# Kernel tuning notes

Measured on AMD Instinct MI355X. Metric: run time of the kernel, lower is better.

The kernel has to match this reference:

```python
import jax, jax.numpy as jnp
import numpy as np

N = 4096  # size of every layer (I, H1, H2, O)
EPS = 1e-5  # torch LayerNorm default


def _ln(x, g, b):
    # torch.nn.LayerNorm: biased variance, affine
    mu = jnp.mean(x)
    xc = x - mu
    v = jnp.mean(xc * xc)
    return xc * jax.lax.rsqrt(v + EPS) * g + b


def setup_inputs() -> dict:
    key = jax.random.key(0)
    ks = jax.random.split(key, 24)
    W = 0.02  # weight scale ~ uniform-init magnitude of nn.Linear at fan_in=4096
    inp = {
        "input_raw": jax.random.normal(ks[0], (N,), jnp.float32),
        "h1_prev": jax.random.normal(ks[1], (N,), jnp.float32),
        "h2_prev": jax.random.normal(ks[2], (N,), jnp.float32),
        "W_I_H1": jax.random.normal(ks[3], (N, N), jnp.float32) * W,
        "W_H1_H1": jax.random.normal(ks[4], (N, N), jnp.float32) * W,
        "W_H1_H2": jax.random.normal(ks[5], (N, N), jnp.float32) * W,
        "W_H2_H1": jax.random.normal(ks[6], (N, N), jnp.float32) * W,
        "W_H2_H2": jax.random.normal(ks[7], (N, N), jnp.float32) * W,
        "W_H1_O": jax.random.normal(ks[8], (N, N), jnp.float32) * W,
        "W_H2_O": jax.random.normal(ks[9], (N, N), jnp.float32) * W,
        "bias_h1": jax.random.normal(ks[10], (N,), jnp.float32) * 0.1,
        "bias_h2": jax.random.normal(ks[11], (N,), jnp.float32) * 0.1,
        "bias_o": jax.random.normal(ks[12], (N,), jnp.float32) * 0.1,
        "g_i": jax.random.uniform(ks[13], (N,), jnp.float32, 0.5, 1.5),
        "b_i": jax.random.normal(ks[14], (N,), jnp.float32) * 0.1,
        "g_h1": jax.random.uniform(ks[15], (N,), jnp.float32, 0.5, 1.5),
        "bln_h1": jax.random.normal(ks[16], (N,), jnp.float32) * 0.1,
        "g_h2": jax.random.uniform(ks[17], (N,), jnp.float32, 0.5, 1.5),
        "bln_h2": jax.random.normal(ks[18], (N,), jnp.float32) * 0.1,
        "g_o": jax.random.uniform(ks[19], (N,), jnp.float32, 0.5, 1.5),
        "bln_o": jax.random.normal(ks[20], (N,), jnp.float32) * 0.1,
    }
    return inp


def reference(input_raw, h1_prev, h2_prev,
              W_I_H1, W_H1_H1, W_H1_H2, W_H2_H1, W_H2_H2, W_H1_O, W_H2_O,
              bias_h1, bias_h2, bias_o,
              g_i, b_i, g_h1, bln_h1, g_h2, bln_h2, g_o, bln_o):
    # --- Phase 1: feedback accumulation + per-layer LayerNorm ---
    # I and O have no feedback -> LN(zeros) = LN bias (beta)
    i_out = b_i + input_raw                       # layers['I']: LN(0) then += input_raw
    h1_fb = _ln(W_H1_H1 @ h1_prev, g_h1, bln_h1)  # self-recurrent feedback H1->H1
    h2_fb = _ln(W_H2_H2 @ h2_prev, g_h2, bln_h2)  # self-recurrent feedback H2->H2
    o_init = bln_o                                # layers['O']: LN(zeros)

    # --- Phase 2: input-driven / feedback-only hidden activations ---
    h1_p2 = jax.nn.relu(_ln(W_I_H1 @ i_out + h1_fb + bias_h1, g_h1, bln_h1))  # 'I' in forward
    h2_p2 = jax.nn.relu(_ln(h2_fb + bias_h2, g_h2, bln_h2))                    # feedback-only

    # --- Phase 3: inter-hidden forward pass (intermediate_output OVERWRITES) ---
    h1_f = jax.nn.relu(_ln(W_H2_H1 @ h2_p2 + bias_h1, g_h1, bln_h1))
    h2_f = jax.nn.relu(_ln(W_H1_H2 @ h1_p2 + bias_h2, g_h2, bln_h2))

    # --- Output layer: sum forwards, tanh(LN(.)) ---
    o = jnp.tanh(_ln(o_init + W_H1_O @ h1_f + W_H2_O @ h2_f + bias_o, g_o, bln_o))
    return o
```

## Files before the change

### kernel.cpp

```cpp
#include <hip/hip_runtime.h>
#include <math.h>

#define NN 4096
#define NV4 1024
#define ROWS_PER_BLOCK 8
#define BLK 256


__device__ __forceinline__ float4 ld4(const float* __restrict__ p, int t) {
    return reinterpret_cast<const float4*>(p)[t];
}
__device__ __forceinline__ void st4(float* __restrict__ p, int t, float4 v) {
    reinterpret_cast<float4*>(p)[t] = v;
}
__device__ __forceinline__ float4 add4(float4 a, float4 b) {
    return make_float4(a.x + b.x, a.y + b.y, a.z + b.z, a.w + b.w);
}

__device__ __forceinline__ float2 block_reduce2(float s, float ss, float* sbuf) {
    #pragma unroll
    for (int off = 32; off > 0; off >>= 1) {
        s  += __shfl_down(s,  off, 64);
        ss += __shfl_down(ss, off, 64);
    }
    const int wave = threadIdx.x >> 6;
    const int lane = threadIdx.x & 63;
    if (lane == 0) { sbuf[wave] = s; sbuf[16 + wave] = ss; }
    __syncthreads();
    float rs = 0.f, rss = 0.f;
    if (threadIdx.x < 16) { rs = sbuf[threadIdx.x]; rss = sbuf[16 + threadIdx.x]; }
    if (wave == 0) {
        #pragma unroll
        for (int off = 8; off > 0; off >>= 1) {
            rs  += __shfl_down(rs,  off, 64);
            rss += __shfl_down(rss, off, 64);
        }
        if (lane == 0) { sbuf[0] = rs; sbuf[1] = rss; }
    }
    __syncthreads();
    float2 r = make_float2(sbuf[0], sbuf[1]);
    __syncthreads();
    return r;
}

struct LNStat { float mu, rstd; };

__device__ __forceinline__ LNStat ln_stats(float4 v, float* sbuf) {
    float s  = v.x + v.y + v.z + v.w;
    float ss = v.x * v.x + v.y * v.y + v.z * v.z + v.w * v.w;
    float2 r = block_reduce2(s, ss, sbuf);
    LNStat o;
    o.mu = r.x * (1.0f / NN);
    float var = r.y * (1.0f / NN) - o.mu * o.mu;
    o.rstd = rsqrtf(var + 1e-5f);
    return o;
}

__device__ __forceinline__ float4 ln_apply(float4 v, LNStat st, float4 g, float4 b) {
    return make_float4((v.x - st.mu) * st.rstd * g.x + b.x,
                       (v.y - st.mu) * st.rstd * g.y + b.y,
                       (v.z - st.mu) * st.rstd * g.z + b.z,
                       (v.w - st.mu) * st.rstd * g.w + b.w);
}

__device__ __forceinline__ float4 relu4(float4 v) {
    return make_float4(fmaxf(v.x, 0.f), fmaxf(v.y, 0.f), fmaxf(v.z, 0.f), fmaxf(v.w, 0.f));
}


__device__ __forceinline__ void gemv8(const float* __restrict__ W,
                                      const float4* __restrict__ xs,
                                      float* __restrict__ y) {
    const int wave = threadIdx.x >> 6;
    const int lane = threadIdx.x & 63;
    const int r0 = blockIdx.x * ROWS_PER_BLOCK + wave * 2;
    const float4* __restrict__ W0 = reinterpret_cast<const float4*>(W + (size_t)r0 * NN);
    const float4* __restrict__ W1 = W0 + NV4;
    float acc0 = 0.f, acc1 = 0.f;
    #pragma unroll
    for (int it = 0; it < 16; ++it) {
        const int j = (it << 6) + lane;
        float4 xv = xs[j];
        float4 a  = W0[j];
        float4 b  = W1[j];
        acc0 = fmaf(a.x, xv.x, acc0);
        acc0 = fmaf(a.y, xv.y, acc0);
        acc0 = fmaf(a.z, xv.z, acc0);
        acc0 = fmaf(a.w, xv.w, acc0);
        acc1 = fmaf(b.x, xv.x, acc1);
        acc1 = fmaf(b.y, xv.y, acc1);
        acc1 = fmaf(b.z, xv.z, acc1);
        acc1 = fmaf(b.w, xv.w, acc1);
    }
    #pragma unroll
    for (int off = 32; off > 0; off >>= 1) {
        acc0 += __shfl_down(acc0, off, 64);
        acc1 += __shfl_down(acc1, off, 64);
    }
    if (lane == 0) { y[r0] = acc0; y[r0 + 1] = acc1; }
}

__global__ __launch_bounds__(BLK) void gemv_stageA(
    const float* __restrict__ W_H1_H1, const float* __restrict__ h1_prev,
    const float* __restrict__ W_H2_H2, const float* __restrict__ h2_prev,
    const float* __restrict__ W_I_H1,  const float* __restrict__ input_raw,
    const float* __restrict__ b_i,
    float* __restrict__ mv1, float* __restrict__ mv2, float* __restrict__ mv3)
{
    __shared__ float4 xs[NV4];
    const float* W; const float* x; const float* xadd; float* y;
    if (blockIdx.y == 0)      { W = W_H1_H1; x = h1_prev;   xadd = nullptr; y = mv1; }
    else if (blockIdx.y == 1) { W = W_H2_H2; x = h2_prev;   xadd = nullptr; y = mv2; }
    else                      { W = W_I_H1;  x = input_raw; xadd = b_i;     y = mv3; }

    const float4* x4 = reinterpret_cast<const float4*>(x);
    if (xadd) {
        const float4* a4 = reinterpret_cast<const float4*>(xadd);
        #pragma unroll
        for (int k = 0; k < 4; ++k) {
            const int j = (k << 8) + threadIdx.x;
            xs[j] = add4(x4[j], a4[j]);
        }
    } else {
        #pragma unroll
        for (int k = 0; k < 4; ++k) {
            const int j = (k << 8) + threadIdx.x;
            xs[j] = x4[j];
        }
    }
    __syncthreads();
    gemv8(W, xs, y);
}

__global__ __launch_bounds__(BLK) void gemv_pair(
    const float* __restrict__ Wa, const float* __restrict__ xa, float* __restrict__ ya,
    const float* __restrict__ Wb, const float* __restrict__ xb, float* __restrict__ yb)
{
    __shared__ float4 xs[NV4];
    const float* W; const float* x; float* y;
    if (blockIdx.y == 0) { W = Wa; x = xa; y = ya; }
    else                 { W = Wb; x = xb; y = yb; }
    const float4* x4 = reinterpret_cast<const float4*>(x);
    #pragma unroll
    for (int k = 0; k < 4; ++k) {
        const int j = (k << 8) + threadIdx.x;
        xs[j] = x4[j];
    }
    __syncthreads();
    gemv8(W, xs, y);
}

__global__ __launch_bounds__(1024) void phase2_kernel(
    const float* __restrict__ mv1, const float* __restrict__ mv2, const float* __restrict__ mv3,
    const float* __restrict__ bias_h1, const float* __restrict__ bias_h2,
    const float* __restrict__ g_h1, const float* __restrict__ bln_h1,
    const float* __restrict__ g_h2, const float* __restrict__ bln_h2,
    float* __restrict__ h1_p2, float* __restrict__ h2_p2)
{
    __shared__ float sbuf[32];
    const int t = threadIdx.x;
    if (blockIdx.x == 0) {
        float4 g = ld4(g_h1, t), b = ld4(bln_h1, t);
        float4 v = ld4(mv1, t);
        LNStat s1 = ln_stats(v, sbuf);
        float4 fb = ln_apply(v, s1, g, b);
        float4 tt = add4(add4(ld4(mv3, t), fb), ld4(bias_h1, t));
        LNStat s2 = ln_stats(tt, sbuf);
        st4(h1_p2, t, relu4(ln_apply(tt, s2, g, b)));
    } else {
        float4 g = ld4(g_h2, t), b = ld4(bln_h2, t);
        float4 v = ld4(mv2, t);
        LNStat s1 = ln_stats(v, sbuf);
        float4 fb = ln_apply(v, s1, g, b);
        float4 tt = add4(fb, ld4(bias_h2, t));
        LNStat s2 = ln_stats(tt, sbuf);
        st4(h2_p2, t, relu4(ln_apply(tt, s2, g, b)));
    }
}

__global__ __launch_bounds__(1024) void phase3_kernel(
    const float* __restrict__ mv4, const float* __restrict__ mv5,
    const float* __restrict__ bias_h1, const float* __restrict__ bias_h2,
    const float* __restrict__ g_h1, const float* __restrict__ bln_h1,
    const float* __restrict__ g_h2, const float* __restrict__ bln_h2,
    float* __restrict__ h1_f, float* __restrict__ h2_f)
{
    __shared__ float sbuf[32];
    const int t = threadIdx.x;
    const float* mv;  const float* bias; const float* g; const float* b; float* out;
    if (blockIdx.x == 0) { mv = mv4; bias = bias_h1; g = g_h1; b = bln_h1; out = h1_f; }
    else                 { mv = mv5; bias = bias_h2; g = g_h2; b = bln_h2; out = h2_f; }
    float4 v = add4(ld4(mv, t), ld4(bias, t));
    LNStat s = ln_stats(v, sbuf);
    st4(out, t, relu4(ln_apply(v, s, ld4(g, t), ld4(b, t))));
}

__global__ __launch_bounds__(1024) void final_kernel(
    const float* __restrict__ mv6, const float* __restrict__ mv7,
    const float* __restrict__ bias_o, const float* __restrict__ bln_o,
    const float* __restrict__ g_o,
    float* __restrict__ out)
{
    __shared__ float sbuf[32];
    const int t = threadIdx.x;
    float4 v = add4(add4(ld4(bln_o, t), ld4(mv6, t)), add4(ld4(mv7, t), ld4(bias_o, t)));
    LNStat s = ln_stats(v, sbuf);
    float4 r = ln_apply(v, s, ld4(g_o, t), ld4(bln_o, t));
    st4(out, t, make_float4(tanhf(r.x), tanhf(r.y), tanhf(r.z), tanhf(r.w)));
}


extern "C" void kernel_launch(void* const* d_in, const int* in_sizes, int n_in,
                              void* d_out, int out_size, void* d_ws, size_t ws_size,
                              hipStream_t stream) {
    const float* input_raw = (const float*)d_in[0];
    const float* h1_prev   = (const float*)d_in[1];
    const float* h2_prev   = (const float*)d_in[2];
    const float* W_I_H1    = (const float*)d_in[3];
    const float* W_H1_H1   = (const float*)d_in[4];
    const float* W_H1_H2   = (const float*)d_in[5];
    const float* W_H2_H1   = (const float*)d_in[6];
    const float* W_H2_H2   = (const float*)d_in[7];
    const float* W_H1_O    = (const float*)d_in[8];
    const float* W_H2_O    = (const float*)d_in[9];
    const float* bias_h1   = (const float*)d_in[10];
    const float* bias_h2   = (const float*)d_in[11];
    const float* bias_o    = (const float*)d_in[12];
    const float* b_i       = (const float*)d_in[14];
    const float* g_h1      = (const float*)d_in[15];
    const float* bln_h1    = (const float*)d_in[16];
    const float* g_h2      = (const float*)d_in[17];
    const float* bln_h2    = (const float*)d_in[18];
    const float* g_o       = (const float*)d_in[19];
    const float* bln_o     = (const float*)d_in[20];

    float* ws    = (float*)d_ws;
    float* mv1   = ws;
    float* mv2   = ws + 1 * NN;
    float* mv3   = ws + 2 * NN;
    float* h1_p2 = ws + 3 * NN;
    float* h2_p2 = ws + 4 * NN;
    float* mv4   = ws + 5 * NN;
    float* mv5   = ws + 6 * NN;
    float* h1_f  = ws + 7 * NN;
    float* h2_f  = ws + 8 * NN;
    float* mv6   = ws + 9 * NN;
    float* mv7   = ws + 10 * NN;

    const int gx = NN / ROWS_PER_BLOCK;

    gemv_stageA<<<dim3(gx, 3), BLK, 0, stream>>>(
        W_H1_H1, h1_prev, W_H2_H2, h2_prev, W_I_H1, input_raw, b_i, mv1, mv2, mv3);

    phase2_kernel<<<2, 1024, 0, stream>>>(
        mv1, mv2, mv3, bias_h1, bias_h2, g_h1, bln_h1, g_h2, bln_h2, h1_p2, h2_p2);

    gemv_pair<<<dim3(gx, 2), BLK, 0, stream>>>(
        W_H2_H1, h2_p2, mv4, W_H1_H2, h1_p2, mv5);

    phase3_kernel<<<2, 1024, 0, stream>>>(
        mv4, mv5, bias_h1, bias_h2, g_h1, bln_h1, g_h2, bln_h2, h1_f, h2_f);

    gemv_pair<<<dim3(gx, 2), BLK, 0, stream>>>(
        W_H1_O, h1_f, mv6, W_H2_O, h2_f, mv7);

    final_kernel<<<1, 1024, 0, stream>>>(
        mv6, mv7, bias_o, bln_o, g_o, (float*)d_out);
}
```

Measured before the change: 104.2 us.

## Compute four rows per wave with batched float4 weight loads in GEMV

Restructures the GEMV inner loop so each wave handles four rows and each thread issues sixteen independent float4 weight loads per iteration before the FMAs. Each block now covers sixteen rows, halving the number of blocks and the redundant staging of the input vector into shared memory. The aim is more memory-level parallelism on the bandwidth-bound weight stream. The trade-off is higher register pressure and fewer blocks to fill the GPU.

New measurement: 114.6 us. 10.0% more time.

```diff
diff --git a/kernel.cpp b/kernel.cpp
--- a/kernel.cpp
+++ b/kernel.cpp
@@ -3,7 +3,8 @@
 
 #define NN 4096
 #define NV4 1024
-#define ROWS_PER_BLOCK 8
+#define RPW 4
+#define ROWS_PER_BLOCK 16
 #define BLK 256
 
 
@@ -68,36 +69,47 @@
 }
 
 
-__device__ __forceinline__ void gemv8(const float* __restrict__ W,
-                                      const float4* __restrict__ xs,
-                                      float* __restrict__ y) {
+__device__ __forceinline__ void gemv16(const float* __restrict__ W,
+                                       const float4* __restrict__ xs,
+                                       float* __restrict__ y) {
     const int wave = threadIdx.x >> 6;
     const int lane = threadIdx.x & 63;
-    const int r0 = blockIdx.x * ROWS_PER_BLOCK + wave * 2;
-    const float4* __restrict__ W0 = reinterpret_cast<const float4*>(W + (size_t)r0 * NN);
-    const float4* __restrict__ W1 = W0 + NV4;
-    float acc0 = 0.f, acc1 = 0.f;
-    #pragma unroll
-    for (int it = 0; it < 16; ++it) {
-        const int j = (it << 6) + lane;
-        float4 xv = xs[j];
-        float4 a  = W0[j];
-        float4 b  = W1[j];
-        acc0 = fmaf(a.x, xv.x, acc0);
-        acc0 = fmaf(a.y, xv.y, acc0);
-        acc0 = fmaf(a.z, xv.z, acc0);
-        acc0 = fmaf(a.w, xv.w, acc0);
-        acc1 = fmaf(b.x, xv.x, acc1);
-        acc1 = fmaf(b.y, xv.y, acc1);
-        acc1 = fmaf(b.z, xv.z, acc1);
-        acc1 = fmaf(b.w, xv.w, acc1);
+    const int r0 = blockIdx.x * ROWS_PER_BLOCK + wave * RPW;
+    const float4* __restrict__ Wr = reinterpret_cast<const float4*>(W) + (size_t)r0 * NV4;
+    float acc[RPW] = {0.f, 0.f, 0.f, 0.f};
+    #pragma unroll
+    for (int it = 0; it < 4; ++it) {
+        const int jb = (it << 8) + lane;
+        float4 w[RPW][4];
+        #pragma unroll
+        for (int r = 0; r < RPW; ++r) {
+            #pragma unroll
+            for (int k = 0; k < 4; ++k)
+                w[r][k] = Wr[(size_t)r * NV4 + jb + (k << 6)];
+        }
+        float4 xv[4];
+        #pragma unroll
+        for (int k = 0; k < 4; ++k) xv[k] = xs[jb + (k << 6)];
+        #pragma unroll
+        for (int r = 0; r < RPW; ++r) {
+            #pragma unroll
+            for (int k = 0; k < 4; ++k) {
+                acc[r] = fmaf(w[r][k].x, xv[k].x, acc[r]);
+                acc[r] = fmaf(w[r][k].y, xv[k].y, acc[r]);
+                acc[r] = fmaf(w[r][k].z, xv[k].z, acc[r]);
+                acc[r] = fmaf(w[r][k].w, xv[k].w, acc[r]);
+            }
+        }
     }
     #pragma unroll
     for (int off = 32; off > 0; off >>= 1) {
-        acc0 += __shfl_down(acc0, off, 64);
-        acc1 += __shfl_down(acc1, off, 64);
-    }
-    if (lane == 0) { y[r0] = acc0; y[r0 + 1] = acc1; }
+        #pragma unroll
+        for (int r = 0; r < RPW; ++r) acc[r] += __shfl_down(acc[r], off, 64);
+    }
+    if (lane == 0) {
+        #pragma unroll
+        for (int r = 0; r < RPW; ++r) y[r0 + r] = acc[r];
+    }
 }
 
 __global__ __launch_bounds__(BLK) void gemv_stageA(
@@ -129,7 +141,7 @@
         }
     }
     __syncthreads();
-    gemv8(W, xs, y);
+    gemv16(W, xs, y);
 }
 
 __global__ __launch_bounds__(BLK) void gemv_pair(
@@ -147,7 +159,7 @@
         xs[j] = x4[j];
     }
     __syncthreads();
-    gemv8(W, xs, y);
+    gemv16(W, xs, y);
 }
 
 __global__ __launch_bounds__(1024) void phase2_kernel(
```

## Double-buffer GEMV weight rows into LDS via async global-to-LDS loads

Applied to the files above, without the earlier changes.

Replaces the register-streaming GEMV with a block-wide loop that stages one weight row at a time into LDS using the global_load_lds builtin. The two LDS buffers are ping-ponged so the next row loads while the current row is dotted against x, which is held in registers. Rows per block double to 16. The aim is to overlap HBM fetches with compute and cut register-held loads. In exchange the loop needs a block barrier per row and 32KB of LDS per block, which may lower occupancy and the number of bytes in flight.

New measurement: 102.4 us. About the same (-1.7%).

```diff
diff --git a/kernel.cpp b/kernel.cpp
--- a/kernel.cpp
+++ b/kernel.cpp
@@ -2,8 +2,7 @@
 #include <math.h>
 
 #define NN 4096
-#define NV4 1024
-#define ROWS_PER_BLOCK 8
+#define ROWS_PER_BLOCK 16
 #define BLK 256
 
 
@@ -15,6 +14,39 @@
 }
 __device__ __forceinline__ float4 add4(float4 a, float4 b) {
     return make_float4(a.x + b.x, a.y + b.y, a.z + b.z, a.w + b.w);
+}
+
+typedef const __attribute__((address_space(1))) unsigned int* gas1_u32;
+typedef __attribute__((address_space(3))) unsigned int* las3_u32;
+__device__ __forceinline__ void async16(const float* g, float* l) {
+    __builtin_amdgcn_global_load_lds((gas1_u32)(const void*)g, (las3_u32)(void*)l, 16, 0, 0);
+}
+
+__device__ __forceinline__ void stage_row(const float* __restrict__ W, int row,
+                                          float* __restrict__ buf, int wave, int lane) {
+    const float* g = W + (size_t)row * NN + wave * 1024 + lane * 4;
+    float* l = buf + wave * 1024;
+    async16(g,       l);
+    async16(g + 256, l + 256);
+    async16(g + 512, l + 512);
+    async16(g + 768, l + 768);
+}
+
+__device__ __forceinline__ float dot_row(const float* __restrict__ buf,
+                                         const float4 xr[4], int tid) {
+    const float4* b4 = reinterpret_cast<const float4*>(buf);
+    float p = 0.f;
+    #pragma unroll
+    for (int i = 0; i < 4; ++i) {
+        float4 w = b4[i * 256 + tid];
+        p = fmaf(w.x, xr[i].x, p);
+        p = fmaf(w.y, xr[i].y, p);
+        p = fmaf(w.z, xr[i].z, p);
+        p = fmaf(w.w, xr[i].w, p);
+    }
+    #pragma unroll
+    for (int off = 32; off > 0; off >>= 1) p += __shfl_down(p, off, 64);
+    return p;
 }
 
 __device__ __forceinline__ float2 block_reduce2(float s, float ss, float* sbuf) {
@@ -68,36 +100,47 @@
 }
 
 
-__device__ __forceinline__ void gemv8(const float* __restrict__ W,
-                                      const float4* __restrict__ xs,
-                                      float* __restrict__ y) {
-    const int wave = threadIdx.x >> 6;
-    const int lane = threadIdx.x & 63;
-    const int r0 = blockIdx.x * ROWS_PER_BLOCK + wave * 2;
-    const float4* __restrict__ W0 = reinterpret_cast<const float4*>(W + (size_t)r0 * NN);
-    const float4* __restrict__ W1 = W0 + NV4;
-    float acc0 = 0.f, acc1 = 0.f;
-    #pragma unroll
-    for (int it = 0; it < 16; ++it) {
-        const int j = (it << 6) + lane;
-        float4 xv = xs[j];
-        float4 a  = W0[j];
-        float4 b  = W1[j];
-        acc0 = fmaf(a.x, xv.x, acc0);
-        acc0 = fmaf(a.y, xv.y, acc0);
-        acc0 = fmaf(a.z, xv.z, acc0);
-        acc0 = fmaf(a.w, xv.w, acc0);
-        acc1 = fmaf(b.x, xv.x, acc1);
-        acc1 = fmaf(b.y, xv.y, acc1);
-        acc1 = fmaf(b.z, xv.z, acc1);
-        acc1 = fmaf(b.w, xv.w, acc1);
-    }
-    #pragma unroll
-    for (int off = 32; off > 0; off >>= 1) {
-        acc0 += __shfl_down(acc0, off, 64);
-        acc1 += __shfl_down(acc1, off, 64);
-    }
-    if (lane == 0) { y[r0] = acc0; y[r0 + 1] = acc1; }
+__device__ __forceinline__ void gemv_core(const float* __restrict__ W,
+                                          const float* __restrict__ x,
+                                          const float* __restrict__ xadd,
+                                          float* __restrict__ y,
+                                          float* t0, float* t1, float* sbuf) {
+    const int tid  = threadIdx.x;
+    const int wave = tid >> 6;
+    const int lane = tid & 63;
+    const int r0 = blockIdx.x * ROWS_PER_BLOCK;
+
+    stage_row(W, r0, t0, wave, lane);
+
+    float4 xr[4];
+    const float4* x4 = reinterpret_cast<const float4*>(x);
+    #pragma unroll
+    for (int i = 0; i < 4; ++i) xr[i] = x4[i * 256 + tid];
+    if (xadd) {
+        const float4* a4 = reinterpret_cast<const float4*>(xadd);
+        #pragma unroll
+        for (int i = 0; i < 4; ++i) xr[i] = add4(xr[i], a4[i * 256 + tid]);
+    }
+    __syncthreads();
+
+    #pragma unroll 1
+    for (int j = 0; j < ROWS_PER_BLOCK; j += 2) {
+        if (tid == 0 && j > 0) y[r0 + j - 1] = sbuf[4] + sbuf[5] + sbuf[6] + sbuf[7];
+        if (j + 1 < ROWS_PER_BLOCK) stage_row(W, r0 + j + 1, t1, wave, lane);
+        {
+            float p = dot_row(t0, xr, tid);
+            if (lane == 0) sbuf[wave] = p;
+        }
+        __syncthreads();
+        if (tid == 0) y[r0 + j] = sbuf[0] + sbuf[1] + sbuf[2] + sbuf[3];
+        if (j + 2 < ROWS_PER_BLOCK) stage_row(W, r0 + j + 2, t0, wave, lane);
+        {
+            float p = dot_row(t1, xr, tid);
+            if (lane == 0) sbuf[4 + wave] = p;
+        }
+        __syncthreads();
+    }
+    if (tid == 0) y[r0 + ROWS_PER_BLOCK - 1] = sbuf[4] + sbuf[5] + sbuf[6] + sbuf[7];
 }
 
 __global__ __launch_bounds__(BLK) void gemv_stageA(
@@ -107,47 +150,25 @@
     const float* __restrict__ b_i,
     float* __restrict__ mv1, float* __restrict__ mv2, float* __restrict__ mv3)
 {
-    __shared__ float4 xs[NV4];
+    __shared__ float t0[NN], t1[NN];
+    __shared__ float sbuf[8];
     const float* W; const float* x; const float* xadd; float* y;
     if (blockIdx.y == 0)      { W = W_H1_H1; x = h1_prev;   xadd = nullptr; y = mv1; }
     else if (blockIdx.y == 1) { W = W_H2_H2; x = h2_prev;   xadd = nullptr; y = mv2; }
     else                      { W = W_I_H1;  x = input_raw; xadd = b_i;     y = mv3; }
-
-    const float4* x4 = reinterpret_cast<const float4*>(x);
-    if (xadd) {
-        const float4* a4 = reinterpret_cast<const float4*>(xadd);
-        #pragma unroll
-        for (int k = 0; k < 4; ++k) {
-            const int j = (k << 8) + threadIdx.x;
-            xs[j] = add4(x4[j], a4[j]);
-        }
-    } else {
-        #pragma unroll
-        for (int k = 0; k < 4; ++k) {
-            const int j = (k << 8) + threadIdx.x;
-            xs[j] = x4[j];
-        }
-    }
-    __syncthreads();
-    gemv8(W, xs, y);
+    gemv_core(W, x, xadd, y, t0, t1, sbuf);
 }
 
 __global__ __launch_bounds__(BLK) void gemv_pair(
     const float* __restrict__ Wa, const float* __restrict__ xa, float* __restrict__ ya,
     const float* __restrict__ Wb, const float* __restrict__ xb, float* __restrict__ yb)
 {
-    __shared__ float4 xs[NV4];
+    __shared__ float t0[NN], t1[NN];
+    __shared__ float sbuf[8];
     const float* W; const float* x; float* y;
     if (blockIdx.y == 0) { W = Wa; x = xa; y = ya; }
     else                 { W = Wb; x = xb; y = yb; }
-    const float4* x4 = reinterpret_cast<const float4*>(x);
-    #pragma unroll
-    for (int k = 0; k < 4; ++k) {
-        const int j = (k << 8) + threadIdx.x;
-        xs[j] = x4[j];
-    }
-    __syncthreads();
-    gemv8(W, xs, y);
+    gemv_core(W, x, nullptr, y, t0, t1, sbuf);
 }
 
 __global__ __launch_bounds__(1024) void phase2_kernel(
```
